# Kernel optimization log

Hardware: AMD Instinct MI355X
Metric: run time of the kernel (lower is better)

Reference implementation:

```python
import jax, jax.numpy as jnp
import numpy as np
from jax import lax

B, S, F, I, D, K, V = 8, 4096, 256, 512, 4, 7, 256  # batch, seq, features, intermediate, depth, kernel, classes


def setup_inputs() -> dict:
    key = jax.random.key(0)
    ks = jax.random.split(key, 7)

    def nrm(k, shape, fan_in):
        return jax.random.normal(k, shape, jnp.float32) / np.float32(np.sqrt(fan_in))

    return {
        "inp": jax.random.randint(ks[0], (B, S), 0, V),
        "emb": nrm(ks[1], (V, 2 * F), F),
        "w0": nrm(ks[2], (D, 3 * I, F, 1), F),          # 1x1 gating conv, features -> 3*intermediate
        "w1": nrm(ks[3], (D, 3 * I, I, K), I * K),       # causal conv, intermediate -> 3*intermediate
        "w2": nrm(ks[4], (D, F, I, 1), I),               # 1x1 conv, intermediate -> features
        "out_w": nrm(ks[5], (V, 2 * F, 1), 2 * F),
        "out_b": jnp.zeros((V,), jnp.float32),
    }


def mish(x):
    return x * jnp.tanh(jax.nn.softplus(x))


def conv1x1(x, w):
    # x: [B, C, S], w: [O, C, 1] -> [B, O, S]
    return jnp.einsum('bcs,oc->bos', x, w[..., 0])


def causal_conv(x, w):
    # x: [B, C, S], w: [O, C, K]; left-pad with K-1 zeros for causality
    k = w.shape[-1]
    xp = jnp.pad(x, ((0, 0), (0, 0), (k - 1, 0)))
    return lax.conv_general_dilated(xp, w, (1,), 'VALID',
                                    dimension_numbers=('NCH', 'OIH', 'NCH'))


def lin_attn(v, divisor):
    # v: [B, 3I, S]; cumsum-normalized linear attention: cumsum(depth)/t * scale + shift
    depth, scale, shift = jnp.split(v, 3, axis=1)
    return jnp.cumsum(depth, axis=-1) / divisor * scale + shift


def cell(x, w0, w1, w2, divisor):
    v = lin_attn(mish(conv1x1(x, w0)), divisor)     # [B, I, S]
    v = lin_attn(mish(causal_conv(v, w1)), divisor) # [B, I, S]
    return conv1x1(v, w2)                            # [B, F, S]


def reference(inp, emb, w0, w1, w2, out_w, out_b):
    divisor = jnp.arange(1, S + 1, dtype=jnp.float32)[None, None, :]  # [1,1,S]
    e = jnp.transpose(emb[inp], (0, 2, 1))  # [B, 2F, S]
    x0, x1 = jnp.split(e, 2, axis=1)
    # reversible residual stack: (x0, x1) -> (x1, x0 + cell(x1))
    for d in range(D):
        x0, x1 = x1, x0 + cell(x1, w0[d], w1[d], w2[d], divisor)
    out = jnp.concatenate([x0, x1], axis=1)  # [B, 2F, S]
    return conv1x1(out, out_w) + out_b[None, :, None]  # [B, V, S]
```

## Files before the change

### kernel.cpp

```cpp
#include <hip/hip_runtime.h>
#include <hip/hip_bf16.h>

#define B_ 8
#define S_ 4096
#define F_ 256
#define I_ 512
#define D_ 4
#define K_ 7
#define V_ 256
#define I3_ 1536
#define KE_ 3584
#define VR_ (S_ + 8)

using bf16 = __hip_bfloat16;
typedef __bf16 bf16x8 __attribute__((ext_vector_type(8)));
typedef float  f32x4  __attribute__((ext_vector_type(4)));

#define LDS_PTR(p) ((__attribute__((address_space(3))) void*)(p))
#define GLB_PTR(p) ((const __attribute__((address_space(1))) void*)(p))

__device__ __forceinline__ float mishf(float x) {
    float u = expf(fminf(x, 30.0f));
    float t = u * (u + 2.0f);
    return x * (t / (t + 2.0f));
}

__device__ __forceinline__ float loadw(const void* p, size_t i, int isbf) {
    return isbf ? __bfloat162float(((const bf16*)p)[i]) : ((const float*)p)[i];
}

__device__ __forceinline__ __bf16 tobf(float x) {
    bf16 h = __float2bfloat16(x);
    return *(__bf16*)&h;
}

__global__ __launch_bounds__(256)
void detect_kernel(int* __restrict__ flag, const unsigned short* __restrict__ p)
{
    __shared__ int sh[256];
    int cnt = 0;
    for (int j = threadIdx.x; j < 16384; j += 256) {
        unsigned int e = (p[j] >> 7) & 0xffu;
        if (e >= 132u) cnt++;
    }
    sh[threadIdx.x] = cnt;
    __syncthreads();
    for (int s = 128; s > 0; s >>= 1) {
        if ((int)threadIdx.x < s) sh[threadIdx.x] += sh[threadIdx.x + s];
        __syncthreads();
    }
    if (threadIdx.x == 0) flag[0] = (sh[0] == 0) ? 1 : 0;
}

__global__ __launch_bounds__(256)
void embed_kernel(float* __restrict__ x0, float* __restrict__ x1,
                  const int* __restrict__ inp, const void* __restrict__ emb,
                  const int* __restrict__ flag)
{
    const int isbf = flag[0];
    size_t idx = (size_t)blockIdx.x * 256 + threadIdx.x;
    int s = (int)(idx % S_);
    int f = (int)((idx / S_) % F_);
    int b = (int)(idx / ((size_t)S_ * F_));
    int tok = inp[b * S_ + s];
    x0[idx] = loadw(emb, (size_t)tok * (2 * F_) + f, isbf);
    x1[idx] = loadw(emb, (size_t)tok * (2 * F_) + F_ + f, isbf);
}

__global__ __launch_bounds__(256)
void cvt_kernel(bf16* __restrict__ dst, const void* __restrict__ src,
                size_t soff, int n, const int* __restrict__ flag)
{
    const int isbf = flag[0];
    int i = blockIdx.x * 256 + threadIdx.x;
    if (i < n) dst[i] = __float2bfloat16(loadw(src, soff + i, isbf));
}

__global__ __launch_bounds__(256)
void zeropad_kernel(bf16* __restrict__ vbt, int nslice)
{
    int i = blockIdx.x * 256 + threadIdx.x;
    if (i < nslice * 6 * I_) {
        int z = i / (6 * I_), off = i % (6 * I_);
        vbt[(size_t)z * VR_ * I_ + off] = __float2bfloat16(0.0f);
    }
}

__global__ __launch_bounds__(256)
void scan_kernel(bf16* __restrict__ vout, const float* __restrict__ t)
{
    const int z = blockIdx.y;
    const int i = blockIdx.x;
    t    += (size_t)z * I3_ * S_;
    vout += (size_t)z * I_ * S_;
    const float* dp  = t + (size_t)i * S_;
    const float* scp = dp + (size_t)I_ * S_;
    const float* shp = dp + (size_t)(2 * I_) * S_;
    bf16* op = vout + (size_t)i * S_;
    const int tid = threadIdx.x;
    const int base = tid * 16;

    float md[16];
    float lsum = 0.f;
    #pragma unroll
    for (int q = 0; q < 4; ++q) {
        float4 dv = *(const float4*)(dp + base + q * 4);
        #pragma unroll
        for (int j = 0; j < 4; ++j) {
            float m = (&dv.x)[j];
            md[q * 4 + j] = m;
            lsum += m;
        }
    }
    float ssum = lsum;
    #pragma unroll
    for (int off = 1; off < 64; off <<= 1) {
        float nv = __shfl_up(ssum, off, 64);
        if ((tid & 63) >= off) ssum += nv;
    }
    __shared__ float wtot[4];
    const int wid = tid >> 6, lane = tid & 63;
    if (lane == 63) wtot[wid] = ssum;
    __syncthreads();
    float excl = ssum - lsum;
    #pragma unroll
    for (int wq = 0; wq < 3; ++wq)
        if (wq < wid) excl += wtot[wq];

    float run = excl;
    bf16x8 o0v, o1v;
    #pragma unroll
    for (int q = 0; q < 4; ++q) {
        float4 scv = *(const float4*)(scp + base + q * 4);
        float4 shv = *(const float4*)(shp + base + q * 4);
        #pragma unroll
        for (int j = 0; j < 4; ++j) {
            run += md[q * 4 + j];
            float sdiv = (float)(base + q * 4 + j + 1);
            float ov = run / sdiv * (&scv.x)[j] + (&shv.x)[j];
            if (q < 2) o0v[q * 4 + j] = tobf(ov);
            else       o1v[(q - 2) * 4 + j] = tobf(ov);
        }
    }
    *(bf16x8*)(void*)(op + base) = o0v;
    *(bf16x8*)(void*)(op + base + 8) = o1v;
}

__global__ __launch_bounds__(256)
void wexp_kernel(bf16* __restrict__ wexp, const void* __restrict__ w1,
                 size_t woff, const int* __restrict__ flag)
{
    const int isbf = flag[0];
    int idx = blockIdx.x * 256 + threadIdx.x;
    int c = idx & 511, o = idx >> 9;
    const size_t base = woff + ((size_t)o * 512 + c) * 7;
    float vals[7];
    #pragma unroll
    for (int k = 0; k < 7; ++k) vals[k] = loadw(w1, base + k, isbf);
    #pragma unroll
    for (int k = 0; k < 7; ++k)
        wexp[(size_t)o * KE_ + (k << 9) + c] = __float2bfloat16(vals[k]);
}

__global__ __launch_bounds__(256)
void trans_kernel(bf16* __restrict__ dst, size_t dzstr,
                  const float* __restrict__ src, size_t szstr, int C)
{
    __shared__ __align__(16) bf16 lt[64][72];
    const int z = blockIdx.z;
    dst += (size_t)z * dzstr;
    src += (size_t)z * szstr;
    const int tid = threadIdx.x;
    const int s0 = blockIdx.x * 64;
    const int c0 = blockIdx.y * 64;
    #pragma unroll
    for (int p = 0; p < 4; ++p) {
        int c = p * 16 + (tid >> 4);
        int sc = (tid & 15) * 4;
        float4 f = *(const float4*)(src + (size_t)(c0 + c) * S_ + s0 + sc);
        #pragma unroll
        for (int j = 0; j < 4; ++j)
            lt[sc + j][c] = __float2bfloat16((&f.x)[j]);
    }
    __syncthreads();
    #pragma unroll
    for (int p = 0; p < 2; ++p) {
        int ch = p * 256 + tid;
        int r = ch >> 3, g = ch & 7;
        *(bf16x8*)(dst + (size_t)(s0 + r) * C + c0 + g * 8) =
            *(const bf16x8*)&lt[r][g * 8];
    }
}

__global__ __launch_bounds__(256)
void transb_kernel(bf16* __restrict__ dst, size_t dzstr,
                   const bf16* __restrict__ src, size_t szstr, int C)
{
    __shared__ __align__(16) bf16 lt[64][72];
    const int z = blockIdx.z;
    dst += (size_t)z * dzstr;
    src += (size_t)z * szstr;
    const int tid = threadIdx.x;
    const int s0 = blockIdx.x * 64;
    const int c0 = blockIdx.y * 64;
    #pragma unroll
    for (int p = 0; p < 2; ++p) {
        int c = p * 32 + (tid >> 3);
        int sc = (tid & 7) * 8;
        bf16x8 v = *(const bf16x8*)(src + (size_t)(c0 + c) * S_ + s0 + sc);
        #pragma unroll
        for (int j = 0; j < 8; ++j)
            *(__bf16*)&lt[sc + j][c] = v[j];
    }
    __syncthreads();
    #pragma unroll
    for (int p = 0; p < 2; ++p) {
        int ch = p * 256 + tid;
        int r = ch >> 3, g = ch & 7;
        *(bf16x8*)(dst + (size_t)(s0 + r) * C + c0 + g * 8) =
            *(const bf16x8*)&lt[r][g * 8];
    }
}

__global__ __launch_bounds__(512, 2)
void gemm128x256_kernel(float* __restrict__ out, size_t ozstr,
                        const bf16* __restrict__ Aw, int lda,
                        const bf16* __restrict__ Bm, size_t bzstr, int ldb,
                        int Kdim, int conv, int domish)
{
    __shared__ __align__(16) bf16 la[3][128][64];
    __shared__ __align__(16) bf16 lb[3][256][64];
    const int tid = threadIdx.x;
    const int s0 = blockIdx.x * 256;
    const int o0 = blockIdx.y * 128;
    const int z  = blockIdx.z;
    out += (size_t)z * ozstr;
    Bm  += (size_t)z * bzstr;
    const int wv = tid >> 6, lane = tid & 63;
    const int wr = wv >> 2, wc = wv & 3;
    const int l16 = lane & 15, q = lane >> 4;
    const int srow = lane >> 3;
    const int schunk = (lane & 7) ^ srow;
    const int nKt = Kdim >> 6;

    f32x4 acc[4][4];
    #pragma unroll
    for (int i = 0; i < 4; ++i)
        #pragma unroll
        for (int j = 0; j < 4; ++j)
            #pragma unroll
            for (int r = 0; r < 4; ++r) acc[i][j][r] = 0.f;

#define STAGE_A3(buf, kt) do {                                                \
    const bf16* gpA_ = Aw + (size_t)(o0 + wv * 8 + srow) * lda                \
                          + ((kt) << 6) + (schunk << 3);                      \
    __builtin_amdgcn_global_load_lds(GLB_PTR(gpA_),                           \
        LDS_PTR(&la[buf][wv * 8][0]), 16, 0, 0);                              \
    __builtin_amdgcn_global_load_lds(GLB_PTR(gpA_ + (size_t)64 * lda),        \
        LDS_PTR(&la[buf][64 + wv * 8][0]), 16, 0, 0);                         \
} while (0)

#define STAGE_BL(buf, l, ro, bk) do {                                         \
    const bf16* gpB_ = Bm + (size_t)(s0 + (l) * 64 + wv * 8 + srow + (ro)) * ldb \
                          + (bk) + (schunk << 3);                             \
    __builtin_amdgcn_global_load_lds(GLB_PTR(gpB_),                           \
        LDS_PTR(&lb[buf][(l) * 64 + wv * 8][0]), 16, 0, 0);                   \
} while (0)

#define LDAF(buf, kk) do {                                                    \
    _Pragma("unroll") for (int i2 = 0; i2 < 4; ++i2) {                        \
        int r_ = wr * 64 + i2 * 16 + l16;                                     \
        af[i2] = *(const bf16x8*)&la[buf][r_][(((kk) * 4 + q) ^ (r_ & 7)) << 3]; \
    }                                                                         \
} while (0)

#define LDBF(buf, kk) do {                                                    \
    _Pragma("unroll") for (int j2 = 0; j2 < 4; ++j2) {                        \
        int r_ = wc * 64 + j2 * 16 + l16;                                     \
        bfr[j2] = *(const bf16x8*)&lb[buf][r_][(((kk) * 4 + q) ^ (r_ & 7)) << 3]; \
    }                                                                         \
} while (0)

#define MFMA16() do {                                                         \
    __builtin_amdgcn_s_setprio(1);                                            \
    _Pragma("unroll") for (int i2 = 0; i2 < 4; ++i2)                          \
    _Pragma("unroll") for (int j2 = 0; j2 < 4; ++j2)                          \
        acc[i2][j2] = __builtin_amdgcn_mfma_f32_16x16x32_bf16(                \
            af[i2], bfr[j2], acc[i2][j2], 0, 0, 0);                           \
    __builtin_amdgcn_s_setprio(0);                                            \
} while (0)

#define BARR()  __builtin_amdgcn_s_barrier()
#define WLGKM() asm volatile("s_waitcnt lgkmcnt(0)" ::: "memory")
#define WVM6()  asm volatile("s_waitcnt vmcnt(6)" ::: "memory")
#define WVM0()  asm volatile("s_waitcnt vmcnt(0)" ::: "memory")

    STAGE_A3(0, 0);
    STAGE_BL(0, 0, 0, 0); STAGE_BL(0, 1, 0, 0);
    STAGE_BL(0, 2, 0, 0); STAGE_BL(0, 3, 0, 0);
    STAGE_A3(1, 1);
    STAGE_BL(1, 0, 0, 64); STAGE_BL(1, 1, 0, 64);
    STAGE_BL(1, 2, 0, 64); STAGE_BL(1, 3, 0, 64);
    WVM6();
    BARR();

    bf16x8 af[4], bfr[4];
    int b = 0;
    for (int t = 0; t < nKt; ++t) {
        int b2 = b + 2; if (b2 >= 3) b2 -= 3;
        const bool st = (t + 2) < nKt;
        int ro2 = 0, bk2 = (t + 2) << 6;
        if (conv) { ro2 = bk2 >> 9; bk2 &= 511; }
        LDAF(b, 0); LDBF(b, 0);
        if (st) { STAGE_A3(b2, t + 2); STAGE_BL(b2, 0, ro2, bk2); }
        BARR(); WLGKM();
        MFMA16();
        BARR();
        LDAF(b, 1); LDBF(b, 1);
        if (st) { STAGE_BL(b2, 1, ro2, bk2); STAGE_BL(b2, 2, ro2, bk2);
                  STAGE_BL(b2, 3, ro2, bk2); }
        BARR(); WLGKM();
        MFMA16();
        if (st) { WVM6(); } else { WVM0(); }
        BARR();
        b += 1; if (b >= 3) b = 0;
    }

    #pragma unroll
    for (int i = 0; i < 4; ++i)
        #pragma unroll
        for (int j = 0; j < 4; ++j) {
            int sg = s0 + wc * 64 + j * 16 + l16;
            #pragma unroll
            for (int r = 0; r < 4; ++r) {
                int og = o0 + wr * 64 + i * 16 + q * 4 + r;
                float v = acc[i][j][r];
                if (domish) v = mishf(v);
                out[(size_t)og * S_ + sg] = v;
            }
        }
#undef STAGE_A3
#undef STAGE_BL
#undef LDAF
#undef LDBF
#undef MFMA16
#undef BARR
#undef WLGKM
#undef WVM6
#undef WVM0
}

__global__ __launch_bounds__(256)
void gemm128_kernel(float* __restrict__ out, size_t ozstr,
                    const bf16* __restrict__ Aw, int lda,
                    const bf16* __restrict__ Bm, size_t bzstr, int ldb,
                    int Kdim, int conv, int addres)
{
    __shared__ __align__(16) bf16 la[128][64];
    __shared__ __align__(16) bf16 lb[128][64];
    const int tid = threadIdx.x;
    const int s0 = blockIdx.x * 128;
    const int o0 = blockIdx.y * 128;
    const int z  = blockIdx.z;
    out += (size_t)z * ozstr;
    Bm  += (size_t)z * bzstr;
    const int wv = tid >> 6, lane = tid & 63;
    const int wo = wv & 1, wsv = wv >> 1;
    const int l16 = lane & 15, q = lane >> 4;
    const int lrow = lane >> 3, lslot = lane & 7;

    f32x4 acc[4][4];
    #pragma unroll
    for (int i = 0; i < 4; ++i)
        #pragma unroll
        for (int j = 0; j < 4; ++j)
            #pragma unroll
            for (int r = 0; r < 4; ++r) acc[i][j][r] = 0.f;

    for (int k0 = 0; k0 < Kdim; k0 += 64) {
        int roff = 0, bk = k0;
        if (conv) { roff = k0 >> 9; bk = k0 & 511; }
        __syncthreads();
        #pragma unroll
        for (int t = 0; t < 4; ++t) {
            int rbase = wv * 32 + t * 8;
            int row = rbase + lrow;
            int chunk = lslot ^ (row & 7);
            __builtin_amdgcn_global_load_lds(
                GLB_PTR(Aw + (size_t)(o0 + row) * lda + k0 + chunk * 8),
                LDS_PTR(&la[rbase][0]), 16, 0, 0);
        }
        #pragma unroll
        for (int t = 0; t < 4; ++t) {
            int rbase = wv * 32 + t * 8;
            int row = rbase + lrow;
            int chunk = lslot ^ (row & 7);
            __builtin_amdgcn_global_load_lds(
                GLB_PTR(Bm + (size_t)(s0 + row + roff) * ldb + bk + chunk * 8),
                LDS_PTR(&lb[rbase][0]), 16, 0, 0);
        }
        __syncthreads();
        #pragma unroll
        for (int kk = 0; kk < 2; ++kk) {
            bf16x8 af[4], bfr[4];
            #pragma unroll
            for (int i = 0; i < 4; ++i) {
                int r = wo * 64 + i * 16 + l16;
                int c = kk * 4 + q;
                af[i] = *(const bf16x8*)&la[r][(c ^ (r & 7)) * 8];
            }
            #pragma unroll
            for (int j = 0; j < 4; ++j) {
                int r = wsv * 64 + j * 16 + l16;
                int c = kk * 4 + q;
                bfr[j] = *(const bf16x8*)&lb[r][(c ^ (r & 7)) * 8];
            }
            #pragma unroll
            for (int i = 0; i < 4; ++i)
                #pragma unroll
                for (int j = 0; j < 4; ++j)
                    acc[i][j] = __builtin_amdgcn_mfma_f32_16x16x32_bf16(
                        af[i], bfr[j], acc[i][j], 0, 0, 0);
        }
    }
    #pragma unroll
    for (int i = 0; i < 4; ++i)
        #pragma unroll
        for (int j = 0; j < 4; ++j) {
            int sg = s0 + wsv * 64 + j * 16 + l16;
            #pragma unroll
            for (int r = 0; r < 4; ++r) {
                int og = o0 + wo * 64 + i * 16 + q * 4 + r;
                float v = acc[i][j][r];
                if (addres) v += out[(size_t)og * S_ + sg];
                out[(size_t)og * S_ + sg] = v;
            }
        }
}

__global__ __launch_bounds__(256)
void final_kernel(void* __restrict__ out, const float* __restrict__ x0,
                  const float* __restrict__ x1, const void* __restrict__ ow,
                  const void* __restrict__ ob, const int* __restrict__ flag)
{
    __shared__ float wl[16][68];
    __shared__ float xl[16][68];
    const int isbf = flag[0];
    const int tid = threadIdx.x;
    const int tx = tid & 15, ty = tid >> 4;
    const int s0 = blockIdx.x * 64;
    const int o0 = blockIdx.y * 64;
    const int b  = blockIdx.z;
    float acc[4][4] = {};
    for (int c0 = 0; c0 < 2 * F_; c0 += 16) {
        if (isbf) {
            #pragma unroll
            for (int e = tid; e < 1024; e += 256) {
                int k = e & 15, o = e >> 4;
                wl[k][o] = __bfloat162float(((const bf16*)ow)[(size_t)(o0 + o) * (2 * F_) + (c0 + k)]);
            }
        } else {
            #pragma unroll
            for (int e = tid; e < 1024; e += 256) {
                int k = e & 15, o = e >> 4;
                wl[k][o] = ((const float*)ow)[(size_t)(o0 + o) * (2 * F_) + (c0 + k)];
            }
        }
        {
            int r = tid >> 4;
            int qq = (tid & 15) * 4;
            int cr = c0 + r;
            const float* src = (cr < F_) ? (x0 + ((size_t)b * F_ + cr) * S_)
                                         : (x1 + ((size_t)b * F_ + (cr - F_)) * S_);
            *(float4*)&xl[r][qq] = *(const float4*)(src + s0 + qq);
        }
        __syncthreads();
        #pragma unroll
        for (int k = 0; k < 16; ++k) {
            float4 av = *(const float4*)&wl[k][ty * 4];
            float4 bv = *(const float4*)&xl[k][tx * 4];
            #pragma unroll
            for (int i = 0; i < 4; ++i)
                #pragma unroll
                for (int j = 0; j < 4; ++j)
                    acc[i][j] += (&av.x)[i] * (&bv.x)[j];
        }
        __syncthreads();
    }
    #pragma unroll
    for (int i = 0; i < 4; ++i) {
        int o = o0 + ty * 4 + i;
        float bias = loadw(ob, o, isbf);
        size_t outoff = ((size_t)b * V_ + o) * S_ + s0 + tx * 4;
        if (isbf) {
            bf16* po = (bf16*)out + outoff;
            #pragma unroll
            for (int j = 0; j < 4; ++j)
                po[j] = __float2bfloat16(acc[i][j] + bias);
        } else {
            float* po = (float*)out + outoff;
            *(float4*)po = make_float4(acc[i][0] + bias, acc[i][1] + bias,
                                       acc[i][2] + bias, acc[i][3] + bias);
        }
    }
}

extern "C" void kernel_launch(void* const* d_in, const int* in_sizes, int n_in,
                              void* d_out, int out_size, void* d_ws, size_t ws_size,
                              hipStream_t stream)
{
    const int*  inp  = (const int*)d_in[0];
    const void* emb  = d_in[1];
    const void* w0   = d_in[2];
    const void* w1   = d_in[3];
    const void* w2   = d_in[4];
    const void* outw = d_in[5];
    const void* outb = d_in[6];

    const size_t NX = (size_t)B_ * F_ * S_;
    const size_t NT = (size_t)I3_ * S_;
    const size_t NV = (size_t)I_ * S_;
    const size_t VSTR = (size_t)VR_ * I_;

    auto need = [&](int p) -> size_t {
        return 256 + 8 * NX + (size_t)4 * p * NT + (size_t)2 * p * NV
             + 2 * ((size_t)I3_ * KE_ + (size_t)p * VSTR + (size_t)p * S_ * F_
                    + (size_t)I3_ * F_ + (size_t)F_ * I_);
    };
    int P = 2;
    if (ws_size >= need(8)) P = 8;
    else if (ws_size >= need(4)) P = 4;

    int*   flag = (int*)d_ws;
    float* A  = (float*)d_ws + 64;
    float* Bb = A + NX;
    float* T  = Bb + NX;
    bf16*  Vv = (bf16*)(T + (size_t)P * NT);
    bf16*  wexp = Vv + (size_t)P * NV;
    bf16*  vbt  = wexp + (size_t)I3_ * KE_;
    bf16*  xbt  = vbt + (size_t)P * VSTR;
    bf16*  wb0  = xbt + (size_t)P * S_ * F_;
    bf16*  wb2  = wb0 + (size_t)I3_ * F_;

    detect_kernel<<<1, 256, 0, stream>>>(flag, (const unsigned short*)emb);
    embed_kernel<<<dim3((unsigned)(NX / 256)), 256, 0, stream>>>(A, Bb, inp, emb, flag);
    zeropad_kernel<<<dim3((P * 6 * I_ + 255) / 256), 256, 0, stream>>>(vbt, P);

    int swap = 0;
    for (int d = 0; d < D_; ++d) {
        wexp_kernel<<<dim3(I3_ * I_ / 256), 256, 0, stream>>>(
            wexp, w1, (size_t)d * I3_ * I_ * K_, flag);
        cvt_kernel<<<dim3(I3_ * F_ / 256), 256, 0, stream>>>(
            wb0, w0, (size_t)d * I3_ * F_, I3_ * F_, flag);
        cvt_kernel<<<dim3(F_ * I_ / 256), 256, 0, stream>>>(
            wb2, w2, (size_t)d * F_ * I_, F_ * I_, flag);
        for (int bp = 0; bp < B_ / P; ++bp) {
            float* x0 = (swap ? Bb : A) + (size_t)(P * bp) * F_ * S_;
            float* x1 = (swap ? A : Bb) + (size_t)(P * bp) * F_ * S_;
            trans_kernel<<<dim3(S_ / 64, F_ / 64, P), 256, 0, stream>>>(
                xbt, (size_t)S_ * F_, x1, (size_t)F_ * S_, F_);
            gemm128x256_kernel<<<dim3(S_ / 256, I3_ / 128, P), 512, 0, stream>>>(
                T, NT, wb0, F_, xbt, (size_t)S_ * F_, F_, F_, 0, 1);
            scan_kernel<<<dim3(I_, P), 256, 0, stream>>>(Vv, T);
            transb_kernel<<<dim3(S_ / 64, I_ / 64, P), 256, 0, stream>>>(
                vbt + 6 * I_, VSTR, Vv, NV, I_);
            gemm128x256_kernel<<<dim3(S_ / 256, I3_ / 128, P), 512, 0, stream>>>(
                T, NT, wexp, KE_, vbt, VSTR, I_, KE_, 1, 1);
            scan_kernel<<<dim3(I_, P), 256, 0, stream>>>(Vv, T);
            transb_kernel<<<dim3(S_ / 64, I_ / 64, P), 256, 0, stream>>>(
                vbt + 6 * I_, VSTR, Vv, NV, I_);
            gemm128_kernel<<<dim3(S_ / 128, F_ / 128, P), 256, 0, stream>>>(
                x0, (size_t)F_ * S_, wb2, I_, vbt + 6 * I_, VSTR, I_, I_, 0, 1);
        }
        swap ^= 1;
    }
    final_kernel<<<dim3(S_ / 64, V_ / 64, B_), 256, 0, stream>>>(d_out, A, Bb, outw, outb, flag);
    (void)in_sizes; (void)n_in; (void)out_size;
}
```

Baseline: 2.929 ms.

## Collapse two half-K phases into one per K-tile, removing intra-tile barriers

The main GEMM loop used to split each 64-wide K tile into two halves, each with its own LDS fragment loads, barrier and lgkmcnt wait. Now all global-to-LDS stages for the tile are issued up front, both K halves of A/B fragments are read into doubled register arrays, and all 32 MFMAs run in one block with only the end-of-iteration barrier. This cuts barrier count and exposes more MFMA work per sync, at the cost of higher register pressure. It also relies on the compiler to insert the LDS waits now that the explicit lgkmcnt wait is gone.

```diff
diff --git a/kernel.cpp b/kernel.cpp
--- a/kernel.cpp
+++ b/kernel.cpp
@@ -267,31 +267,35 @@
         LDS_PTR(&lb[buf][(l) * 64 + wv * 8][0]), 16, 0, 0);                   \
 } while (0)
 
-#define LDAF(buf, kk) do {                                                    \
-    _Pragma("unroll") for (int i2 = 0; i2 < 4; ++i2) {                        \
+#define LDAF8(buf) do {                                                       \
+    _Pragma("unroll") for (int i2 = 0; i2 < 4; ++i2)                          \
+    _Pragma("unroll") for (int kk = 0; kk < 2; ++kk) {                        \
         int r_ = wr * 64 + i2 * 16 + l16;                                     \
-        af[i2] = *(const bf16x8*)&la[buf][r_][(((kk) * 4 + q) ^ (r_ & 7)) << 3]; \
+        af[i2 * 2 + kk] =                                                     \
+            *(const bf16x8*)&la[buf][r_][((kk * 4 + q) ^ (r_ & 7)) << 3];     \
     }                                                                         \
 } while (0)
 
-#define LDBF(buf, kk) do {                                                    \
-    _Pragma("unroll") for (int j2 = 0; j2 < 4; ++j2) {                        \
+#define LDBF8(buf) do {                                                       \
+    _Pragma("unroll") for (int j2 = 0; j2 < 4; ++j2)                          \
+    _Pragma("unroll") for (int kk = 0; kk < 2; ++kk) {                        \
         int r_ = wc * 64 + j2 * 16 + l16;                                     \
-        bfr[j2] = *(const bf16x8*)&lb[buf][r_][(((kk) * 4 + q) ^ (r_ & 7)) << 3]; \
+        bfr[j2 * 2 + kk] =                                                    \
+            *(const bf16x8*)&lb[buf][r_][((kk * 4 + q) ^ (r_ & 7)) << 3];     \
     }                                                                         \
 } while (0)
 
-#define MFMA16() do {                                                         \
+#define MFMA32() do {                                                         \
     __builtin_amdgcn_s_setprio(1);                                            \
+    _Pragma("unroll") for (int kk = 0; kk < 2; ++kk)                          \
     _Pragma("unroll") for (int i2 = 0; i2 < 4; ++i2)                          \
     _Pragma("unroll") for (int j2 = 0; j2 < 4; ++j2)                          \
         acc[i2][j2] = __builtin_amdgcn_mfma_f32_16x16x32_bf16(                \
-            af[i2], bfr[j2], acc[i2][j2], 0, 0, 0);                           \
+            af[i2 * 2 + kk], bfr[j2 * 2 + kk], acc[i2][j2], 0, 0, 0);         \
     __builtin_amdgcn_s_setprio(0);                                            \
 } while (0)
 
 #define BARR()  __builtin_amdgcn_s_barrier()
-#define WLGKM() asm volatile("s_waitcnt lgkmcnt(0)" ::: "memory")
 #define WVM6()  asm volatile("s_waitcnt vmcnt(6)" ::: "memory")
 #define WVM0()  asm volatile("s_waitcnt vmcnt(0)" ::: "memory")
 
@@ -304,23 +308,20 @@
     WVM6();
     BARR();
 
-    bf16x8 af[4], bfr[4];
+    bf16x8 af[8], bfr[8];
     int b = 0;
     for (int t = 0; t < nKt; ++t) {
         int b2 = b + 2; if (b2 >= 3) b2 -= 3;
         const bool st = (t + 2) < nKt;
         int ro2 = 0, bk2 = (t + 2) << 6;
         if (conv) { ro2 = bk2 >> 9; bk2 &= 511; }
-        LDAF(b, 0); LDBF(b, 0);
-        if (st) { STAGE_A3(b2, t + 2); STAGE_BL(b2, 0, ro2, bk2); }
-        BARR(); WLGKM();
-        MFMA16();
-        BARR();
-        LDAF(b, 1); LDBF(b, 1);
-        if (st) { STAGE_BL(b2, 1, ro2, bk2); STAGE_BL(b2, 2, ro2, bk2);
-                  STAGE_BL(b2, 3, ro2, bk2); }
-        BARR(); WLGKM();
-        MFMA16();
+        if (st) {
+            STAGE_A3(b2, t + 2);
+            STAGE_BL(b2, 0, ro2, bk2); STAGE_BL(b2, 1, ro2, bk2);
+            STAGE_BL(b2, 2, ro2, bk2); STAGE_BL(b2, 3, ro2, bk2);
+        }
+        LDAF8(b); LDBF8(b);
+        MFMA32();
         if (st) { WVM6(); } else { WVM0(); }
         BARR();
         b += 1; if (b >= 3) b = 0;
@@ -341,11 +342,10 @@
         }
 #undef STAGE_A3
 #undef STAGE_BL
-#undef LDAF
-#undef LDBF
-#undef MFMA16
+#undef LDAF8
+#undef LDBF8
+#undef MFMA32
 #undef BARR
-#undef WLGKM
 #undef WVM6
 #undef WVM0
 }
```

New measurement: 3.270 ms. +11.7%, slower.

## Enlarge GEMM tile to 192x256 with double buffering for more reuse

Applied to the files above, without the earlier changes.

The main GEMM tile grows from 128x256 to 192x256 outputs per block, so each wave now holds 6x4 accumulators and B tiles are reused across more output rows. To fit the larger A tile in LDS, the triple-buffered pipeline becomes double-buffered with a one-step prefetch, interleaved across four MFMA phases and waiting on vmcnt(0) every iteration. Occupancy drops to one block per CU, and the shallower prefetch may expose more memory latency. The grid along the output dimension shrinks from 12 to 8 blocks.

```diff
diff --git a/kernel.cpp b/kernel.cpp
--- a/kernel.cpp
+++ b/kernel.cpp
@@ -222,17 +222,17 @@
     }
 }
 
-__global__ __launch_bounds__(512, 2)
-void gemm128x256_kernel(float* __restrict__ out, size_t ozstr,
-                        const bf16* __restrict__ Aw, int lda,
-                        const bf16* __restrict__ Bm, size_t bzstr, int ldb,
-                        int Kdim, int conv, int domish)
-{
-    __shared__ __align__(16) bf16 la[3][128][64];
-    __shared__ __align__(16) bf16 lb[3][256][64];
+__global__ __launch_bounds__(512, 1)
+void gemm192_kernel(float* __restrict__ out, size_t ozstr,
+                    const bf16* __restrict__ Aw, int lda,
+                    const bf16* __restrict__ Bm, size_t bzstr, int ldb,
+                    int Kdim, int conv, int domish)
+{
+    __shared__ __align__(16) bf16 la[2][192][64];
+    __shared__ __align__(16) bf16 lb[2][256][64];
     const int tid = threadIdx.x;
     const int s0 = blockIdx.x * 256;
-    const int o0 = blockIdx.y * 128;
+    const int o0 = blockIdx.y * 192;
     const int z  = blockIdx.z;
     out += (size_t)z * ozstr;
     Bm  += (size_t)z * bzstr;
@@ -243,9 +243,9 @@
     const int schunk = (lane & 7) ^ srow;
     const int nKt = Kdim >> 6;
 
-    f32x4 acc[4][4];
-    #pragma unroll
-    for (int i = 0; i < 4; ++i)
+    f32x4 acc[6][4];
+    #pragma unroll
+    for (int i = 0; i < 6; ++i)
         #pragma unroll
         for (int j = 0; j < 4; ++j)
             #pragma unroll
@@ -258,6 +258,8 @@
         LDS_PTR(&la[buf][wv * 8][0]), 16, 0, 0);                              \
     __builtin_amdgcn_global_load_lds(GLB_PTR(gpA_ + (size_t)64 * lda),        \
         LDS_PTR(&la[buf][64 + wv * 8][0]), 16, 0, 0);                         \
+    __builtin_amdgcn_global_load_lds(GLB_PTR(gpA_ + (size_t)128 * lda),       \
+        LDS_PTR(&la[buf][128 + wv * 8][0]), 16, 0, 0);                        \
 } while (0)
 
 #define STAGE_BL(buf, l, ro, bk) do {                                         \
@@ -267,73 +269,75 @@
         LDS_PTR(&lb[buf][(l) * 64 + wv * 8][0]), 16, 0, 0);                   \
 } while (0)
 
-#define LDAF(buf, kk) do {                                                    \
-    _Pragma("unroll") for (int i2 = 0; i2 < 4; ++i2) {                        \
-        int r_ = wr * 64 + i2 * 16 + l16;                                     \
+#define LDAF3(buf, kk, ih) do {                                               \
+    _Pragma("unroll") for (int i2 = 0; i2 < 3; ++i2) {                        \
+        int r_ = wr * 96 + (ih) * 48 + i2 * 16 + l16;                         \
         af[i2] = *(const bf16x8*)&la[buf][r_][(((kk) * 4 + q) ^ (r_ & 7)) << 3]; \
     }                                                                         \
 } while (0)
 
-#define LDBF(buf, kk) do {                                                    \
+#define LDBF4(buf, kk) do {                                                   \
     _Pragma("unroll") for (int j2 = 0; j2 < 4; ++j2) {                        \
         int r_ = wc * 64 + j2 * 16 + l16;                                     \
         bfr[j2] = *(const bf16x8*)&lb[buf][r_][(((kk) * 4 + q) ^ (r_ & 7)) << 3]; \
     }                                                                         \
 } while (0)
 
-#define MFMA16() do {                                                         \
+#define MFMA12(ih) do {                                                       \
     __builtin_amdgcn_s_setprio(1);                                            \
-    _Pragma("unroll") for (int i2 = 0; i2 < 4; ++i2)                          \
+    _Pragma("unroll") for (int i2 = 0; i2 < 3; ++i2)                          \
     _Pragma("unroll") for (int j2 = 0; j2 < 4; ++j2)                          \
-        acc[i2][j2] = __builtin_amdgcn_mfma_f32_16x16x32_bf16(                \
-            af[i2], bfr[j2], acc[i2][j2], 0, 0, 0);                           \
+        acc[(ih) * 3 + i2][j2] = __builtin_amdgcn_mfma_f32_16x16x32_bf16(     \
+            af[i2], bfr[j2], acc[(ih) * 3 + i2][j2], 0, 0, 0);                \
     __builtin_amdgcn_s_setprio(0);                                            \
 } while (0)
 
 #define BARR()  __builtin_amdgcn_s_barrier()
 #define WLGKM() asm volatile("s_waitcnt lgkmcnt(0)" ::: "memory")
-#define WVM6()  asm volatile("s_waitcnt vmcnt(6)" ::: "memory")
 #define WVM0()  asm volatile("s_waitcnt vmcnt(0)" ::: "memory")
 
     STAGE_A3(0, 0);
     STAGE_BL(0, 0, 0, 0); STAGE_BL(0, 1, 0, 0);
     STAGE_BL(0, 2, 0, 0); STAGE_BL(0, 3, 0, 0);
-    STAGE_A3(1, 1);
-    STAGE_BL(1, 0, 0, 64); STAGE_BL(1, 1, 0, 64);
-    STAGE_BL(1, 2, 0, 64); STAGE_BL(1, 3, 0, 64);
-    WVM6();
+    WVM0();
     BARR();
 
-    bf16x8 af[4], bfr[4];
-    int b = 0;
+    bf16x8 af[3], bfr[4];
     for (int t = 0; t < nKt; ++t) {
-        int b2 = b + 2; if (b2 >= 3) b2 -= 3;
-        const bool st = (t + 2) < nKt;
-        int ro2 = 0, bk2 = (t + 2) << 6;
-        if (conv) { ro2 = bk2 >> 9; bk2 &= 511; }
-        LDAF(b, 0); LDBF(b, 0);
-        if (st) { STAGE_A3(b2, t + 2); STAGE_BL(b2, 0, ro2, bk2); }
+        const int c = t & 1, n = c ^ 1;
+        const bool st = (t + 1) < nKt;
+        int ro1 = 0, bk1 = (t + 1) << 6;
+        if (conv) { ro1 = bk1 >> 9; bk1 &= 511; }
+        LDAF3(c, 0, 0); LDBF4(c, 0);
+        if (st) STAGE_A3(n, t + 1);
         BARR(); WLGKM();
-        MFMA16();
+        MFMA12(0);
         BARR();
-        LDAF(b, 1); LDBF(b, 1);
-        if (st) { STAGE_BL(b2, 1, ro2, bk2); STAGE_BL(b2, 2, ro2, bk2);
-                  STAGE_BL(b2, 3, ro2, bk2); }
+        LDAF3(c, 0, 1);
+        if (st) { STAGE_BL(n, 0, ro1, bk1); STAGE_BL(n, 1, ro1, bk1); }
         BARR(); WLGKM();
-        MFMA16();
-        if (st) { WVM6(); } else { WVM0(); }
+        MFMA12(1);
         BARR();
-        b += 1; if (b >= 3) b = 0;
-    }
-
-    #pragma unroll
-    for (int i = 0; i < 4; ++i)
+        LDAF3(c, 1, 0); LDBF4(c, 1);
+        if (st) { STAGE_BL(n, 2, ro1, bk1); STAGE_BL(n, 3, ro1, bk1); }
+        BARR(); WLGKM();
+        MFMA12(0);
+        BARR();
+        LDAF3(c, 1, 1);
+        BARR(); WLGKM();
+        MFMA12(1);
+        WVM0();
+        BARR();
+    }
+
+    #pragma unroll
+    for (int i = 0; i < 6; ++i)
         #pragma unroll
         for (int j = 0; j < 4; ++j) {
             int sg = s0 + wc * 64 + j * 16 + l16;
             #pragma unroll
             for (int r = 0; r < 4; ++r) {
-                int og = o0 + wr * 64 + i * 16 + q * 4 + r;
+                int og = o0 + wr * 96 + i * 16 + q * 4 + r;
                 float v = acc[i][j][r];
                 if (domish) v = mishf(v);
                 out[(size_t)og * S_ + sg] = v;
@@ -341,12 +345,11 @@
         }
 #undef STAGE_A3
 #undef STAGE_BL
-#undef LDAF
-#undef LDBF
-#undef MFMA16
+#undef LDAF3
+#undef LDBF4
+#undef MFMA12
 #undef BARR
 #undef WLGKM
-#undef WVM6
 #undef WVM0
 }
 
@@ -559,12 +562,12 @@
             float* x1 = (swap ? A : Bb) + (size_t)(P * bp) * F_ * S_;
             trans_kernel<<<dim3(S_ / 64, F_ / 64, P), 256, 0, stream>>>(
                 xbt, (size_t)S_ * F_, x1, (size_t)F_ * S_, F_);
-            gemm128x256_kernel<<<dim3(S_ / 256, I3_ / 128, P), 512, 0, stream>>>(
+            gemm192_kernel<<<dim3(S_ / 256, I3_ / 192, P), 512, 0, stream>>>(
                 T, NT, wb0, F_, xbt, (size_t)S_ * F_, F_, F_, 0, 1);
             scan_kernel<<<dim3(I_, P), 256, 0, stream>>>(Vv, T);
             transb_kernel<<<dim3(S_ / 64, I_ / 64, P), 256, 0, stream>>>(
                 vbt + 6 * I_, VSTR, Vv, NV, I_);
-            gemm128x256_kernel<<<dim3(S_ / 256, I3_ / 128, P), 512, 0, stream>>>(
+            gemm192_kernel<<<dim3(S_ / 256, I3_ / 192, P), 512, 0, stream>>>(
                 T, NT, wexp, KE_, vbt, VSTR, I_, KE_, 1, 1);
             scan_kernel<<<dim3(I_, P), 256, 0, stream>>>(Vv, T);
             transb_kernel<<<dim3(S_ / 64, I_ / 64, P), 256, 0, stream>>>(
```

Result: faster. 2.822 ms (-3.7%).
